# Optimization experiments

Hardware: AMD Instinct MI355X
Metric: run time of the kernel (lower is better)

## Reference

```python
import jax, jax.numpy as jnp
import numpy as np

N_HEADS = 16
CONTEXT_WINDOW = 256


def _band_mask(s_q, s_k):
    # True = masked out. Module (causal=True, context_window=256) allows only
    # keys with 0 <= (query_pos - key_pos) < CONTEXT_WINDOW (causal mask is
    # subsumed by the lower band).
    d = jnp.arange(s_q)[:, None] - jnp.arange(s_k)[None, :]
    return ~((d >= 0) & (d < CONTEXT_WINDOW))


def setup_inputs() -> dict:
    key = jax.random.key(0)
    ks = jax.random.split(key, 5)
    B, S, D = 2, 2048, 1024
    std = 0.02
    return {
        "query": jax.random.normal(ks[0], (B, S, D), dtype=jnp.float32),
        "Wq": jax.random.normal(ks[1], (D, D), dtype=jnp.float32) * std,
        "bq": jnp.zeros((D,), dtype=jnp.float32),
        "Wk": jax.random.normal(ks[2], (D, D), dtype=jnp.float32) * std,
        "bk": jnp.zeros((D,), dtype=jnp.float32),
        "Wv": jax.random.normal(ks[3], (D, D), dtype=jnp.float32) * std,
        "bv": jnp.zeros((D,), dtype=jnp.float32),
        "Wo": jax.random.normal(ks[4], (D, D), dtype=jnp.float32) * std,
        "bo": jnp.zeros((D,), dtype=jnp.float32),
    }


def reference(query, Wq, bq, Wk, bk, Wv, bv, Wo, bo):
    B, S, D = query.shape
    H = N_HEADS
    Dh = D // H
    # projections -> [B, H, S, Dh]
    q = (query @ Wq + bq).reshape(B, S, H, Dh).transpose(0, 2, 1, 3)
    k = (query @ Wk + bk).reshape(B, S, H, Dh).transpose(0, 2, 1, 3)
    v = (query @ Wv + bv).reshape(B, S, H, Dh).transpose(0, 2, 1, 3)
    scores = jnp.einsum("bhqd,bhkd->bhqk", q, k) * (1.0 / np.sqrt(Dh))
    mask = _band_mask(S, S)  # [S, S]
    scores = jnp.where(mask[None, None, :, :], -jnp.inf, scores)
    attn = jax.nn.softmax(scores, axis=-1)
    out = jnp.einsum("bhqk,bhkd->bhqd", attn, v)
    out = out.transpose(0, 2, 1, 3).reshape(B, S, D)
    return out @ Wo + bo
```

## Files before the change

kernel.cpp:

```cpp
#include <hip/hip_runtime.h>
#include <hip/hip_bf16.h>


typedef __bf16 bf16x8 __attribute__((ext_vector_type(8)));
typedef float f32x4 __attribute__((ext_vector_type(4)));
typedef short s16x4 __attribute__((ext_vector_type(4)));
typedef unsigned short u16x8 __attribute__((ext_vector_type(8)));
typedef unsigned short u16x4 __attribute__((ext_vector_type(4)));

__device__ __forceinline__ unsigned short f2bf(float f) {
  unsigned int u = __builtin_bit_cast(unsigned int, f);
  u += 0x7FFFu + ((u >> 16) & 1u);
  return (unsigned short)(u >> 16);
}

__device__ __forceinline__ f32x4 mfma32(bf16x8 a, bf16x8 b, f32x4 c) {
  return __builtin_amdgcn_mfma_f32_16x16x32_bf16(a, b, c, 0, 0, 0);
}
__device__ __forceinline__ f32x4 mfma16(s16x4 a, s16x4 b, f32x4 c) {
  return __builtin_amdgcn_mfma_f32_16x16x16bf16_1k(a, b, c, 0, 0, 0);
}

__device__ __forceinline__ void gl16(const unsigned short* gsrc,
                                     unsigned short* lds) {
  __builtin_amdgcn_global_load_lds(
      (const __attribute__((address_space(1))) unsigned int*)gsrc,
      (__attribute__((address_space(3))) unsigned int*)lds, 16, 0, 0);
}

__global__ __launch_bounds__(256) void cvt_all(
    const float* __restrict__ x,
    const float* __restrict__ Wq, const float* __restrict__ Wk,
    const float* __restrict__ Wv, const float* __restrict__ Wo,
    unsigned short* __restrict__ xb, unsigned short* __restrict__ Wt) {
  const int z = blockIdx.z;
  const int tx = threadIdx.x, ty = threadIdx.y;
  if (z == 4) {
    const int tid = (blockIdx.y * 32 + blockIdx.x) * 256 + ty * 32 + tx;
#pragma unroll
    for (int it = 0; it < 4; ++it) {
      const int i = tid + it * 262144;
      const float4 v = ((const float4*)x)[i];
      u16x4 o = { f2bf(v.x), f2bf(v.y), f2bf(v.z), f2bf(v.w) };
      *(u16x4*)(xb + (size_t)i * 4) = o;
    }
    return;
  }
  const float* W = (z == 0) ? Wq : (z == 1) ? Wk : (z == 2) ? Wv : Wo;
  unsigned short* dst = Wt + (size_t)z * 1024 * 1024;
  __shared__ float t[32][33];
  const int n0 = blockIdx.x * 32, k0 = blockIdx.y * 32;
#pragma unroll
  for (int i = 0; i < 32; i += 8)
    t[ty + i][tx] = W[(size_t)(k0 + ty + i) * 1024 + n0 + tx];
  __syncthreads();
#pragma unroll
  for (int i = 0; i < 32; i += 8)
    dst[(size_t)(n0 + ty + i) * 1024 + k0 + tx] = f2bf(t[tx][ty + i]);
}

__global__ __launch_bounds__(512, 2) void gemm_qkv(
    const unsigned short* __restrict__ A, const unsigned short* __restrict__ Bt,
    const float* __restrict__ bq, const float* __restrict__ bk,
    const float* __restrict__ bv,
    unsigned short* __restrict__ q_ws, unsigned short* __restrict__ k_ws,
    unsigned short* __restrict__ v_ws) {
  __shared__ __align__(16) unsigned short Alds[3][8192];
  __shared__ __align__(16) unsigned short Blds[3][8192];
  const int tid = threadIdx.x, lane = tid & 63, w = tid >> 6;
  const int lq = lane & 15, lg = lane >> 4;
  const int bm = blockIdx.x, bn = blockIdx.y;
  const int wr = (w >> 2) * 128, wc = (w & 3) * 64;

  const int srow = tid >> 2;
  const int scs = ((tid & 3) ^ ((tid >> 3) & 3)) << 3;
  const unsigned short* Ag = A + (size_t)(bm * 256 + srow) * 1024 + scs;
  const unsigned short* Bg = Bt + (size_t)(bn * 256 + srow) * 1024 + scs;

  auto stageA = [&](int kt2, int s2, int i) {
    gl16(Ag + (size_t)i * 128 * 1024 + kt2, &Alds[s2][i * 4096 + w * 512]);
  };
  auto stageB = [&](int kt2, int s2, int i) {
    gl16(Bg + (size_t)i * 128 * 1024 + kt2, &Blds[s2][i * 4096 + w * 512]);
  };

  const int cs = (lq >> 1) & 3;
  auto rdA = [&](int s, int m) {
    return *(const bf16x8*)(&Alds[s][(wr + m * 16 + lq) * 32 +
                                     ((lg ^ cs) << 3)]);
  };
  auto rdB = [&](int s, int n) {
    return *(const bf16x8*)(&Blds[s][(wc + n * 16 + lq) * 32 +
                                     ((lg ^ cs) << 3)]);
  };

  f32x4 acc[8][4] = {};
  stageA(0, 0, 0); stageA(0, 0, 1); stageB(0, 0, 0); stageB(0, 0, 1);
  stageA(32, 1, 0); stageA(32, 1, 1); stageB(32, 1, 0); stageB(32, 1, 1);

  int s = 0;
  for (int t = 0; t < 32; ++t) {
    if (t < 31) asm volatile("s_waitcnt vmcnt(4)" ::: "memory");
    else        asm volatile("s_waitcnt vmcnt(0)" ::: "memory");
    asm volatile("s_barrier" ::: "memory");
    const int kt2 = (t + 2) * 32;
    const int s2 = (s == 0) ? 2 : s - 1;
    const bool st = (t < 30);
    bf16x8 am[4], bf[4];
    if (st) stageA(kt2, s2, 0);
#pragma unroll
    for (int m = 0; m < 4; ++m) am[m] = rdA(s, m);
    bf[0] = rdB(s, 0); bf[1] = rdB(s, 1);
    __builtin_amdgcn_s_setprio(1);
#pragma unroll
    for (int m = 0; m < 4; ++m) {
      acc[m][0] = mfma32(am[m], bf[0], acc[m][0]);
      acc[m][1] = mfma32(am[m], bf[1], acc[m][1]);
    }
    __builtin_amdgcn_s_setprio(0);
    if (st) stageA(kt2, s2, 1);
    bf[2] = rdB(s, 2); bf[3] = rdB(s, 3);
    __builtin_amdgcn_s_setprio(1);
#pragma unroll
    for (int m = 0; m < 4; ++m) {
      acc[m][2] = mfma32(am[m], bf[2], acc[m][2]);
      acc[m][3] = mfma32(am[m], bf[3], acc[m][3]);
    }
    __builtin_amdgcn_s_setprio(0);
    if (st) stageB(kt2, s2, 0);
#pragma unroll
    for (int m = 0; m < 4; ++m) am[m] = rdA(s, m + 4);
    __builtin_amdgcn_s_setprio(1);
#pragma unroll
    for (int m = 0; m < 4; ++m) {
      acc[m + 4][0] = mfma32(am[m], bf[0], acc[m + 4][0]);
      acc[m + 4][1] = mfma32(am[m], bf[1], acc[m + 4][1]);
    }
    __builtin_amdgcn_s_setprio(0);
    if (st) stageB(kt2, s2, 1);
    __builtin_amdgcn_s_setprio(1);
#pragma unroll
    for (int m = 0; m < 4; ++m) {
      acc[m + 4][2] = mfma32(am[m], bf[2], acc[m + 4][2]);
      acc[m + 4][3] = mfma32(am[m], bf[3], acc[m + 4][3]);
    }
    __builtin_amdgcn_s_setprio(0);
    s = (s == 2) ? 0 : s + 1;
  }

  const int ttype = bn >> 2;
  const float* bias = (ttype == 0) ? bq : (ttype == 1) ? bk : bv;
  unsigned short* dst = (ttype == 0) ? q_ws : (ttype == 1) ? k_ws : v_ws;
  const float scalef = (ttype == 0) ? 0.125f : 1.0f;
  const int ccb = (bn & 3) * 256 + wc + lq;
  const int r0 = bm * 256 + wr + lg * 4;
#pragma unroll
  for (int m = 0; m < 8; ++m) {
#pragma unroll
    for (int n = 0; n < 4; ++n) {
      const int cc = ccb + n * 16;
      const int h = cc >> 6, dh = cc & 63;
#pragma unroll
      for (int j = 0; j < 4; ++j) {
        const int row = r0 + m * 16 + j;
        const int b = row >> 11, sq = row & 2047;
        const float v = (acc[m][n][j] + bias[cc]) * scalef;
        dst[((size_t)(b * 16 + h) * 2048 + sq) * 64 + dh] = f2bf(v);
      }
    }
  }
}

__global__ __launch_bounds__(256) void gemm_out(
    const unsigned short* __restrict__ A, const unsigned short* __restrict__ Bt,
    const float* __restrict__ bo, float* __restrict__ outp) {
  __shared__ unsigned short Alds[128 * 32];
  __shared__ unsigned short Blds[64 * 32];
  const int tid = threadIdx.x, lane = tid & 63, w = tid >> 6;
  const int lq = lane & 15, lg = lane >> 4;
  const int bm = blockIdx.x, bn = blockIdx.y;
  const int wr = (w >> 1) * 64, wc = (w & 1) * 32;

  const int srow = lane >> 2, scol8 = (lane & 3) * 8;
  const unsigned short* Ag =
      A + (size_t)(bm * 128 + w * 32 + srow) * 1024 + scol8;
  const unsigned short* Bg =
      Bt + (size_t)(bn * 64 + w * 16 + srow) * 1024 + scol8;
  unsigned short* Al0 = Alds + (w * 32) * 32;
  unsigned short* Al1 = Alds + (w * 32 + 16) * 32;
  unsigned short* Bl0 = Blds + (w * 16) * 32;

  f32x4 acc[4][2] = {};
  for (int kt = 0; kt < 1024; kt += 32) {
    __syncthreads();
    gl16(Ag + kt, Al0);
    gl16(Ag + kt + 16 * 1024, Al1);
    gl16(Bg + kt, Bl0);
    __syncthreads();
    bf16x8 af[4], bfr[2];
#pragma unroll
    for (int m = 0; m < 4; ++m)
      af[m] = *(const bf16x8*)(Alds + (wr + m * 16 + lq) * 32 + lg * 8);
#pragma unroll
    for (int n = 0; n < 2; ++n)
      bfr[n] = *(const bf16x8*)(Blds + (wc + n * 16 + lq) * 32 + lg * 8);
#pragma unroll
    for (int m = 0; m < 4; ++m)
#pragma unroll
      for (int n = 0; n < 2; ++n)
        acc[m][n] = mfma32(af[m], bfr[n], acc[m][n]);
  }

  const int r0 = bm * 128 + wr + lg * 4;
  const int c0g = bn * 64 + wc + lq;
#pragma unroll
  for (int m = 0; m < 4; ++m)
#pragma unroll
    for (int n = 0; n < 2; ++n) {
      const int col = c0g + n * 16;
#pragma unroll
      for (int j = 0; j < 4; ++j)
        outp[(size_t)(r0 + m * 16 + j) * 1024 + col] = acc[m][n][j] + bo[col];
    }
}

__global__ __launch_bounds__(256) void attn_kernel(
    const unsigned short* __restrict__ q_ws,
    const unsigned short* __restrict__ k_ws,
    const unsigned short* __restrict__ v_ws,
    unsigned short* __restrict__ attn_out) {
  __shared__ unsigned short o_lds[4][16 * 64];
  const int tid = threadIdx.x, lane = tid & 63, w = tid >> 6;
  const int lq = lane & 15, lg = lane >> 4;
  const int bh = blockIdx.y;
  const int q0 = blockIdx.x * 64 + w * 16;
  const unsigned short* Q = q_ws + (size_t)bh * 2048 * 64;
  const unsigned short* Kp = k_ws + (size_t)bh * 2048 * 64;
  const unsigned short* Vp = v_ws + (size_t)bh * 2048 * 64;

  const bf16x8 qf0 = *(const bf16x8*)(Q + (size_t)(q0 + lq) * 64 + lg * 8);
  const bf16x8 qf1 = *(const bf16x8*)(Q + (size_t)(q0 + lq) * 64 + 32 + lg * 8);

  float lsum = 0.f;
  f32x4 oacc[4] = {};
  int t0 = (q0 - 255) >> 4;
  if (t0 < 0) t0 = 0;
  const int t1 = q0 >> 4;

  for (int t = t0; t <= t1; ++t) {
    const int j0 = t * 16;
    const bf16x8 kf0 = *(const bf16x8*)(Kp + (size_t)(j0 + lq) * 64 + lg * 8);
    const bf16x8 kf1 =
        *(const bf16x8*)(Kp + (size_t)(j0 + lq) * 64 + 32 + lg * 8);
    f32x4 stv = {};
    stv = mfma32(kf0, qf0, stv);
    stv = mfma32(kf1, qf1, stv);

    float p[4], ps = 0.f;
#pragma unroll
    for (int r = 0; r < 4; ++r) {
      const int delta = (q0 + lq) - (j0 + lg * 4 + r);
      const bool ok = (delta >= 0) && (delta < 256);
      p[r] = ok ? __expf(stv[r] - 4.0f) : 0.f;
      ps += p[r];
    }
    ps += __shfl_xor(ps, 16);
    ps += __shfl_xor(ps, 32);
    lsum += ps;

    s16x4 pb = { (short)f2bf(p[0]), (short)f2bf(p[1]),
                 (short)f2bf(p[2]), (short)f2bf(p[3]) };
#pragma unroll
    for (int c = 0; c < 4; ++c) {
      s16x4 vf;
#pragma unroll
      for (int j = 0; j < 4; ++j)
        vf[j] = (short)Vp[(size_t)(j0 + lg * 4 + j) * 64 + c * 16 + lq];
      oacc[c] = mfma16(vf, pb, oacc[c]);
    }
  }

  const float rl = 1.f / lsum;
#pragma unroll
  for (int c = 0; c < 4; ++c)
#pragma unroll
    for (int r = 0; r < 4; ++r)
      o_lds[w][lq * 64 + c * 16 + lg * 4 + r] = f2bf(oacc[c][r] * rl);
  __syncthreads();
  const int row = lane >> 2, d0 = (lane & 3) * 16;
  const u16x8 o0 = *(const u16x8*)(&o_lds[w][row * 64 + d0]);
  const u16x8 o1 = *(const u16x8*)(&o_lds[w][row * 64 + d0 + 8]);
  const size_t g =
      ((size_t)((bh >> 4) * 2048 + q0 + row)) * 1024 + (bh & 15) * 64 + d0;
  *(u16x8*)(attn_out + g) = o0;
  *(u16x8*)(attn_out + g + 8) = o1;
}

extern "C" void kernel_launch(void* const* d_in, const int* in_sizes, int n_in,
                              void* d_out, int out_size, void* d_ws,
                              size_t ws_size, hipStream_t stream) {
  const float* query = (const float*)d_in[0];
  const float* Wq = (const float*)d_in[1];
  const float* bq = (const float*)d_in[2];
  const float* Wk = (const float*)d_in[3];
  const float* bk = (const float*)d_in[4];
  const float* Wv = (const float*)d_in[5];
  const float* bv = (const float*)d_in[6];
  const float* Wo = (const float*)d_in[7];
  const float* bo = (const float*)d_in[8];
  float* outp = (float*)d_out;

  char* ws = (char*)d_ws;
  unsigned short* xbf = (unsigned short*)(ws);
  unsigned short* wt  = (unsigned short*)(ws + (8u << 20));
  unsigned short* qws = (unsigned short*)(ws + (16u << 20));
  unsigned short* kws = (unsigned short*)(ws + (24u << 20));
  unsigned short* vws = (unsigned short*)(ws + (32u << 20));

  cvt_all<<<dim3(32, 32, 5), dim3(32, 8), 0, stream>>>(query, Wq, Wk, Wv, Wo,
                                                       xbf, wt);
  gemm_qkv<<<dim3(16, 12), 512, 0, stream>>>(xbf, wt, bq, bk, bv, qws, kws,
                                             vws);
  attn_kernel<<<dim3(32, 32), 256, 0, stream>>>(qws, kws, vws, xbf);
  gemm_out<<<dim3(32, 16), 256, 0, stream>>>(
      xbf, wt + (size_t)3 * 1024 * 1024, bo, outp);
}
```

Before: 103.3 us.

## Retile QKV GEMM to 256x128 tiles with 4 waves and barrier-phased schedule

The QKV projection GEMM moves from 256x256 tiles with 8 waves to 256x128 tiles with 4 waves, doubling the grid from 192 to 384 blocks so more of the CUs are filled. The main loop is rescheduled into phases split by explicit s_barrier and lgkmcnt waits, with each global-to-LDS load interleaved between MFMA clusters and the vmcnt wait moved to the end of the iteration. The aim is better CU occupancy and overlap of loads with MFMA work. In exchange, each block reuses its A tile across fewer columns and runs many more barriers per iteration.

```diff
diff --git a/kernel.cpp b/kernel.cpp
--- a/kernel.cpp
+++ b/kernel.cpp
@@ -26,6 +26,13 @@
   __builtin_amdgcn_global_load_lds(
       (const __attribute__((address_space(1))) unsigned int*)gsrc,
       (__attribute__((address_space(3))) unsigned int*)lds, 16, 0, 0);
+}
+
+__device__ __forceinline__ void rawbar() {
+  asm volatile("s_barrier" ::: "memory");
+}
+__device__ __forceinline__ void lgkm0() {
+  asm volatile("s_waitcnt lgkmcnt(0)" ::: "memory");
 }
 
 __global__ __launch_bounds__(256) void cvt_all(
@@ -59,29 +66,29 @@
     dst[(size_t)(n0 + ty + i) * 1024 + k0 + tx] = f2bf(t[tx][ty + i]);
 }
 
-__global__ __launch_bounds__(512, 2) void gemm_qkv(
+__global__ __launch_bounds__(256, 2) void gemm_qkv(
     const unsigned short* __restrict__ A, const unsigned short* __restrict__ Bt,
     const float* __restrict__ bq, const float* __restrict__ bk,
     const float* __restrict__ bv,
     unsigned short* __restrict__ q_ws, unsigned short* __restrict__ k_ws,
     unsigned short* __restrict__ v_ws) {
   __shared__ __align__(16) unsigned short Alds[3][8192];
-  __shared__ __align__(16) unsigned short Blds[3][8192];
+  __shared__ __align__(16) unsigned short Blds[3][4096];
   const int tid = threadIdx.x, lane = tid & 63, w = tid >> 6;
   const int lq = lane & 15, lg = lane >> 4;
   const int bm = blockIdx.x, bn = blockIdx.y;
-  const int wr = (w >> 2) * 128, wc = (w & 3) * 64;
-
-  const int srow = tid >> 2;
-  const int scs = ((tid & 3) ^ ((tid >> 3) & 3)) << 3;
+  const int wr = (w >> 1) * 128, wc = (w & 1) * 64;
+
+  const int srow = w * 16 + (lane >> 2);
+  const int scs = ((lane & 3) ^ ((lane >> 3) & 3)) << 3;
   const unsigned short* Ag = A + (size_t)(bm * 256 + srow) * 1024 + scs;
-  const unsigned short* Bg = Bt + (size_t)(bn * 256 + srow) * 1024 + scs;
+  const unsigned short* Bg = Bt + (size_t)(bn * 128 + srow) * 1024 + scs;
 
   auto stageA = [&](int kt2, int s2, int i) {
-    gl16(Ag + (size_t)i * 128 * 1024 + kt2, &Alds[s2][i * 4096 + w * 512]);
+    gl16(Ag + (size_t)i * 64 * 1024 + kt2, &Alds[s2][i * 2048 + w * 512]);
   };
   auto stageB = [&](int kt2, int s2, int i) {
-    gl16(Bg + (size_t)i * 128 * 1024 + kt2, &Blds[s2][i * 4096 + w * 512]);
+    gl16(Bg + (size_t)i * 64 * 1024 + kt2, &Blds[s2][i * 2048 + w * 512]);
   };
 
   const int cs = (lq >> 1) & 3;
@@ -95,22 +102,23 @@
   };
 
   f32x4 acc[8][4] = {};
-  stageA(0, 0, 0); stageA(0, 0, 1); stageB(0, 0, 0); stageB(0, 0, 1);
-  stageA(32, 1, 0); stageA(32, 1, 1); stageB(32, 1, 0); stageB(32, 1, 1);
+  stageA(0, 0, 0); stageA(0, 0, 1); stageA(0, 0, 2); stageA(0, 0, 3);
+  stageB(0, 0, 0); stageB(0, 0, 1);
+  stageA(32, 1, 0); stageA(32, 1, 1); stageA(32, 1, 2); stageA(32, 1, 3);
+  stageB(32, 1, 0); stageB(32, 1, 1);
+  asm volatile("s_waitcnt vmcnt(6)" ::: "memory");
+  rawbar();
 
   int s = 0;
   for (int t = 0; t < 32; ++t) {
-    if (t < 31) asm volatile("s_waitcnt vmcnt(4)" ::: "memory");
-    else        asm volatile("s_waitcnt vmcnt(0)" ::: "memory");
-    asm volatile("s_barrier" ::: "memory");
     const int kt2 = (t + 2) * 32;
     const int s2 = (s == 0) ? 2 : s - 1;
     const bool st = (t < 30);
-    bf16x8 am[4], bf[4];
-    if (st) stageA(kt2, s2, 0);
-#pragma unroll
-    for (int m = 0; m < 4; ++m) am[m] = rdA(s, m);
+    bf16x8 am[4], am2[4], bf[4];
+    if (st) { stageA(kt2, s2, 0); stageA(kt2, s2, 1); }
+    am[0] = rdA(s, 0); am[1] = rdA(s, 1); am[2] = rdA(s, 2); am[3] = rdA(s, 3);
     bf[0] = rdB(s, 0); bf[1] = rdB(s, 1);
+    rawbar(); lgkm0();
     __builtin_amdgcn_s_setprio(1);
 #pragma unroll
     for (int m = 0; m < 4; ++m) {
@@ -118,8 +126,11 @@
       acc[m][1] = mfma32(am[m], bf[1], acc[m][1]);
     }
     __builtin_amdgcn_s_setprio(0);
-    if (st) stageA(kt2, s2, 1);
+    rawbar();
+    if (st) { stageA(kt2, s2, 2); stageA(kt2, s2, 3); }
     bf[2] = rdB(s, 2); bf[3] = rdB(s, 3);
+    am2[0] = rdA(s, 4); am2[1] = rdA(s, 5);
+    rawbar(); lgkm0();
     __builtin_amdgcn_s_setprio(1);
 #pragma unroll
     for (int m = 0; m < 4; ++m) {
@@ -127,32 +138,38 @@
       acc[m][3] = mfma32(am[m], bf[3], acc[m][3]);
     }
     __builtin_amdgcn_s_setprio(0);
+    rawbar();
     if (st) stageB(kt2, s2, 0);
-#pragma unroll
-    for (int m = 0; m < 4; ++m) am[m] = rdA(s, m + 4);
+    am2[2] = rdA(s, 6); am2[3] = rdA(s, 7);
+    rawbar(); lgkm0();
     __builtin_amdgcn_s_setprio(1);
 #pragma unroll
-    for (int m = 0; m < 4; ++m) {
-      acc[m + 4][0] = mfma32(am[m], bf[0], acc[m + 4][0]);
-      acc[m + 4][1] = mfma32(am[m], bf[1], acc[m + 4][1]);
+    for (int n = 0; n < 4; ++n) {
+      acc[4][n] = mfma32(am2[0], bf[n], acc[4][n]);
+      acc[5][n] = mfma32(am2[1], bf[n], acc[5][n]);
     }
     __builtin_amdgcn_s_setprio(0);
+    rawbar();
     if (st) stageB(kt2, s2, 1);
+    rawbar();
     __builtin_amdgcn_s_setprio(1);
 #pragma unroll
-    for (int m = 0; m < 4; ++m) {
-      acc[m + 4][2] = mfma32(am[m], bf[2], acc[m + 4][2]);
-      acc[m + 4][3] = mfma32(am[m], bf[3], acc[m + 4][3]);
+    for (int n = 0; n < 4; ++n) {
+      acc[6][n] = mfma32(am2[2], bf[n], acc[6][n]);
+      acc[7][n] = mfma32(am2[3], bf[n], acc[7][n]);
     }
     __builtin_amdgcn_s_setprio(0);
+    if (t < 30) asm volatile("s_waitcnt vmcnt(6)" ::: "memory");
+    else if (t == 30) asm volatile("s_waitcnt vmcnt(0)" ::: "memory");
+    rawbar();
     s = (s == 2) ? 0 : s + 1;
   }
 
-  const int ttype = bn >> 2;
+  const int ttype = bn >> 3;
   const float* bias = (ttype == 0) ? bq : (ttype == 1) ? bk : bv;
   unsigned short* dst = (ttype == 0) ? q_ws : (ttype == 1) ? k_ws : v_ws;
   const float scalef = (ttype == 0) ? 0.125f : 1.0f;
-  const int ccb = (bn & 3) * 256 + wc + lq;
+  const int ccb = (bn & 7) * 128 + wc + lq;
   const int r0 = bm * 256 + wr + lg * 4;
 #pragma unroll
   for (int m = 0; m < 8; ++m) {
@@ -319,7 +336,7 @@
 
   cvt_all<<<dim3(32, 32, 5), dim3(32, 8), 0, stream>>>(query, Wq, Wk, Wv, Wo,
                                                        xbf, wt);
-  gemm_qkv<<<dim3(16, 12), 512, 0, stream>>>(xbf, wt, bq, bk, bv, qws, kws,
+  gemm_qkv<<<dim3(16, 24), 256, 0, stream>>>(xbf, wt, bq, bk, bv, qws, kws,
                                              vws);
   attn_kernel<<<dim3(32, 32), 256, 0, stream>>>(qws, kws, vws, xbf);
   gemm_out<<<dim3(32, 16), 256, 0, stream>>>(
```

Measured after the change: 105.5 us. +2.1%, slower.
